# Optimization experiments

Measured on AMD Instinct MI355X. Metric: run time of the kernel, lower is better.

Reference implementation:

```python
import jax, jax.numpy as jnp
import numpy as np

EMBED = 1024
HEADS = 16
HEAD_DIM = EMBED // HEADS
B, T = 2, 2048
ROPE_THETA = 10000.0


def _rope(x):
    # x: [B, H, T, D]; standard half-split rotary embedding, applied per head
    D = x.shape[-1]
    inv_freq = 1.0 / (ROPE_THETA ** (jnp.arange(0, D, 2, dtype=jnp.float32) / D))  # [D/2]
    freqs = jnp.arange(x.shape[2], dtype=jnp.float32)[:, None] * inv_freq[None, :]  # [T, D/2]
    cos = jnp.cos(freqs).astype(x.dtype)  # [T, D/2]
    sin = jnp.sin(freqs).astype(x.dtype)
    x1, x2 = x[..., : D // 2], x[..., D // 2 :]
    return jnp.concatenate([x1 * cos - x2 * sin, x2 * cos + x1 * sin], axis=-1)


def setup_inputs() -> dict:
    key = jax.random.key(0)
    ks = jax.random.split(key, 5)
    s = 1.0 / np.sqrt(EMBED)
    return {
        "x": jax.random.normal(ks[0], (B, T, EMBED), dtype=jnp.float32),
        "Wq": jax.random.normal(ks[1], (EMBED, EMBED), dtype=jnp.float32) * s,
        "bq": jnp.zeros((EMBED,), dtype=jnp.float32),
        "Wk": jax.random.normal(ks[2], (EMBED, EMBED), dtype=jnp.float32) * s,
        "bk": jnp.zeros((EMBED,), dtype=jnp.float32),
        "Wv": jax.random.normal(ks[3], (EMBED, EMBED), dtype=jnp.float32) * s,
        "bv": jnp.zeros((EMBED,), dtype=jnp.float32),
        "Wo": jax.random.normal(ks[4], (EMBED, EMBED), dtype=jnp.float32) * s,
        "bo": jnp.zeros((EMBED,), dtype=jnp.float32),
    }


def reference(x, Wq, bq, Wk, bk, Wv, bv, Wo, bo):
    Bb, Tt, C = x.shape
    H, D = HEADS, HEAD_DIM
    # torch Linear: y = x @ W.T + b
    def proj(W, b):
        return (jnp.einsum("btc,oc->bto", x, W) + b).reshape(Bb, Tt, H, D).transpose(0, 2, 1, 3)

    q = _rope(proj(Wq, bq))  # [B, H, T, D]
    k = _rope(proj(Wk, bk))
    v = proj(Wv, bv)
    scale = jnp.sqrt(jnp.asarray(D, dtype=x.dtype))
    scores = jnp.einsum("bhtd,bhsd->bhts", q, k) / scale  # [B, H, T, T]
    attn = jax.nn.softmax(scores, axis=-1)  # dropout = identity in eval mode
    out = jnp.einsum("bhts,bhsd->bhtd", attn, v)  # [B, H, T, D]
    out = out.transpose(0, 2, 1, 3).reshape(Bb, Tt, C)
    return jnp.einsum("btc,oc->bto", out, Wo) + bo
```

## Files before the change

### kernel.cpp

```cpp
#include <hip/hip_runtime.h>
#include <hip/hip_bf16.h>

#define EMBED 1024
#define HEADS 16
#define HDIM 64
#define BATCH 2
#define SEQ 2048
#define MTOT (BATCH*SEQ)

typedef __attribute__((ext_vector_type(2))) float f32x2;
typedef __attribute__((ext_vector_type(4))) float f32x4;
typedef __attribute__((ext_vector_type(16))) float f32x16;
typedef __attribute__((ext_vector_type(4))) short s16x4;
typedef __attribute__((ext_vector_type(8))) short bf16x8;
typedef __attribute__((ext_vector_type(4))) int i32x4;

static __device__ __forceinline__ short f2bf(float f) {
  unsigned u = __builtin_bit_cast(unsigned, f);
  unsigned r = (u + 0x7fffu + ((u >> 16) & 1u)) >> 16;
  return (short)r;
}
static __device__ __forceinline__ float bf2f(short s) {
  unsigned u = ((unsigned)(unsigned short)s) << 16;
  return __builtin_bit_cast(float, u);
}
static __device__ __forceinline__ int pack2bf_fast(float lo, float hi) {
  unsigned ulo = __builtin_bit_cast(unsigned, lo) + 0x8000u;
  unsigned uhi = __builtin_bit_cast(unsigned, hi) + 0x8000u;
  int r;
  asm("v_cvt_pk_bf16_f32 %0, %1, %2" : "=v"(r)
      : "v"(__builtin_bit_cast(float, ulo)), "v"(__builtin_bit_cast(float, uhi)));
  return r;
}
static __device__ __forceinline__ void pswap(int &a, int &b) {
  asm("v_permlane32_swap_b32 %0, %1" : "+v"(a), "+v"(b));
}

typedef __attribute__((address_space(1))) const void gvoid_t;
typedef __attribute__((address_space(3))) void lvoid_t;
static __device__ __forceinline__ void gload_lds16(const void* g, void* l) {
  __builtin_amdgcn_global_load_lds((gvoid_t*)g, (lvoid_t*)l, 16, 0, 0);
}

__global__ __launch_bounds__(256) void cvt_bf16(
    const float* __restrict__ x,
    const float* __restrict__ Wq, const float* __restrict__ Wk,
    const float* __restrict__ Wv, const float* __restrict__ Wo,
    short* __restrict__ xb,
    short* __restrict__ Wqb, short* __restrict__ Wkb,
    short* __restrict__ Wvb, short* __restrict__ Wob,
    f32x2* __restrict__ tab)
{
  int i = blockIdx.x * 256 + threadIdx.x;
  if (i >= 2097152) {
    int i2 = i - 2097152;
    int t = i2 >> 5, j = i2 & 31;
    float invf = exp2f(-(float)j * 0.4152410118609203f);
    float sn, cs;
    sincosf((float)t * invf, &sn, &cs);
    f32x2 e; e[0] = cs; e[1] = sn;
    tab[i2] = e;
    return;
  }
  const float* src; short* dst; int off;
  if (i < 1048576) { src = x; dst = xb; off = i; }
  else {
    int j = i - 1048576;
    int w = j >> 18; off = j & 262143;
    src = (w == 0) ? Wq : (w == 1) ? Wk : (w == 2) ? Wv : Wo;
    dst = (w == 0) ? Wqb : (w == 1) ? Wkb : (w == 2) ? Wvb : Wob;
  }
  f32x4 v = ((const f32x4*)src)[off];
  s16x4 h;
#pragma unroll
  for (int j = 0; j < 4; ++j) h[j] = f2bf(v[j]);
  ((s16x4*)dst)[off] = h;
}

__global__ __launch_bounds__(256) void qkv_gemm(
    const short* __restrict__ xb,
    const short* __restrict__ Wqb, const short* __restrict__ Wkb, const short* __restrict__ Wvb,
    const float* __restrict__ bq, const float* __restrict__ bk, const float* __restrict__ bv,
    const f32x2* __restrict__ tab,
    short* __restrict__ Qb, short* __restrict__ Kb, short* __restrict__ Vb)
{
  __shared__ short As[128][64];
  __shared__ short Bs[128][64];
  int tid = threadIdx.x;
  int lane = tid & 63, wid = tid >> 6;
  int wm = wid >> 1, wn = wid & 1;
  int bm = blockIdx.x / 24;
  int bncol = blockIdx.x % 24;
  int wsel = bncol >> 3, bnn = bncol & 7;
  const short* W    = (wsel == 0) ? Wqb : (wsel == 1) ? Wkb : Wvb;
  const float* bias = (wsel == 0) ? bq : (wsel == 1) ? bk : bv;

  f32x4 acc[4][4] = {};

  const short* Abase = xb + (size_t)bm * 128 * EMBED;
  const short* Bbase = W + (size_t)bnn * 128 * EMBED;
  char* AsB = (char*)&As[0][0];
  char* BsB = (char*)&Bs[0][0];

  for (int kt = 0; kt < EMBED / 64; ++kt) {
#pragma unroll
    for (int i = 0; i < 4; ++i) {
      int s = tid + i * 256;
      int row = s >> 3, c = s & 7;
      int cs = c ^ (row & 7);
      gload_lds16(&Abase[(size_t)row * EMBED + kt * 64 + cs * 8],
                  AsB + i * 4096 + wid * 1024 + lane * 16);
      gload_lds16(&Bbase[(size_t)row * EMBED + kt * 64 + cs * 8],
                  BsB + i * 4096 + wid * 1024 + lane * 16);
    }
    __syncthreads();
#pragma unroll
    for (int kk = 0; kk < 2; ++kk) {
      int cp = ((kk * 4 + (lane >> 4)) ^ (lane & 7)) * 8;
      bf16x8 af[4], bfr[4];
#pragma unroll
      for (int mf = 0; mf < 4; ++mf)
        af[mf] = *(const bf16x8*)&As[wm * 64 + mf * 16 + (lane & 15)][cp];
#pragma unroll
      for (int nf = 0; nf < 4; ++nf)
        bfr[nf] = *(const bf16x8*)&Bs[wn * 64 + nf * 16 + (lane & 15)][cp];
      if (wsel == 2) {
#pragma unroll
        for (int mf = 0; mf < 4; ++mf)
#pragma unroll
          for (int nf = 0; nf < 4; ++nf)
            acc[mf][nf] = __builtin_amdgcn_mfma_f32_16x16x32_bf16(bfr[mf], af[nf], acc[mf][nf], 0, 0, 0);
      } else {
#pragma unroll
        for (int mf = 0; mf < 4; ++mf)
#pragma unroll
          for (int nf = 0; nf < 4; ++nf)
            acc[mf][nf] = __builtin_amdgcn_mfma_f32_16x16x32_bf16(af[mf], bfr[nf], acc[mf][nf], 0, 0, 0);
      }
    }
    __syncthreads();
  }

  if (wsel < 2) {
    short* dst = (wsel == 0) ? Qb : Kb;
    float sc = (wsel == 0) ? 0.18033688011112042f : 1.0f;
#pragma unroll
    for (int nf = 0; nf < 2; ++nf) {
      int col = bnn * 128 + wn * 64 + nf * 16 + (lane & 15);
      int h = col >> 6, j = col & 31;
      float b1 = bias[col], b2 = bias[col + 32];
#pragma unroll
      for (int mf = 0; mf < 4; ++mf) {
        int row0 = bm * 128 + wm * 64 + mf * 16 + ((lane >> 4) << 2);
#pragma unroll
        for (int r = 0; r < 4; ++r) {
          int m = row0 + r;
          int b_ = m >> 11, t = m & (SEQ - 1);
          f32x2 e = tab[t * 32 + j];
          float a1 = acc[mf][nf][r] + b1;
          float a2 = acc[mf][nf + 2][r] + b2;
          size_t o = (((size_t)(b_ * HEADS + h)) * SEQ + t) * HDIM + j;
          dst[o]      = f2bf((a1 * e[0] - a2 * e[1]) * sc);
          dst[o + 32] = f2bf((a2 * e[0] + a1 * e[1]) * sc);
        }
      }
    }
  } else {
#pragma unroll
    for (int mf = 0; mf < 4; ++mf) {
#pragma unroll
      for (int r = 0; r < 4; ++r) {
        int cch = bnn * 128 + wn * 64 + mf * 16 + ((lane >> 4) << 2) + r;
        int h = cch >> 6, d = cch & 63;
        float bb = bias[cch];
#pragma unroll
        for (int nf = 0; nf < 4; ++nf) {
          int m = bm * 128 + wm * 64 + nf * 16 + (lane & 15);
          int b_ = m >> 11, t = m & (SEQ - 1);
          Vb[((size_t)(b_ * HEADS + h) * HDIM + d) * SEQ + t] = f2bf(acc[mf][nf][r] + bb);
        }
      }
    }
  }
}

#define QBLK 128
#define KBLK 128

__global__ __launch_bounds__(256, 2) void attn_kernel(
    const short* __restrict__ Qb, const short* __restrict__ Kb,
    const short* __restrict__ Vb, short* __restrict__ Ob)
{
  __shared__ short Ks[KBLK][68];
  __shared__ short Vs[HDIM][132];

  int tid = threadIdx.x, lane = tid & 63, wid = tid >> 6;
  int l31 = lane & 31, lhi = lane >> 5;

  int bid = blockIdx.x;
  int swz = (bid & 7) * 64 + (bid >> 3);
  int qi = swz & 15, bh = swz >> 4;
  int b = bh >> 4, h = bh & 15;

  const short* Qp = Qb + ((size_t)bh * SEQ + qi * QBLK + wid * 32) * HDIM;
  const short* Kp = Kb + (size_t)bh * SEQ * HDIM;
  const short* Vp = Vb + (size_t)bh * HDIM * SEQ;

  bf16x8 qf[4];
#pragma unroll
  for (int cc = 0; cc < 4; ++cc)
    qf[cc] = *(const bf16x8*)&Qp[(size_t)l31 * HDIM + cc * 16 + lhi * 8];

  f32x16 oacc0 = {}, oacc1 = {}, lacc = {};
  bf16x8 vones;
#pragma unroll
  for (int j = 0; j < 8; ++j) vones[j] = (short)0x3F80;

  bf16x8 kreg[4], vreg[4];
#pragma unroll
  for (int i = 0; i < 4; ++i) {
    int s = tid + i * 256;
    kreg[i] = *(const bf16x8*)&Kp[(size_t)(s >> 3) * HDIM + (s & 7) * 8];
    vreg[i] = *(const bf16x8*)&Vp[(size_t)(s >> 4) * SEQ + (s & 15) * 8];
  }

  for (int kt = 0; kt < SEQ / KBLK; ++kt) {
#pragma unroll
    for (int i = 0; i < 4; ++i) {
      int s = tid + i * 256;
      *(bf16x8*)&Ks[s >> 3][(s & 7) * 8] = kreg[i];
      *(bf16x8*)&Vs[s >> 4][(s & 15) * 8] = vreg[i];
    }
    __syncthreads();

    if (kt + 1 < SEQ / KBLK) {
#pragma unroll
      for (int i = 0; i < 4; ++i) {
        int s = tid + i * 256;
        kreg[i] = *(const bf16x8*)&Kp[(size_t)((kt + 1) * KBLK + (s >> 3)) * HDIM + (s & 7) * 8];
        vreg[i] = *(const bf16x8*)&Vp[(size_t)(s >> 4) * SEQ + (kt + 1) * KBLK + (s & 15) * 8];
      }
    }

#pragma unroll
    for (int kbp = 0; kbp < 4; kbp += 2) {
      f32x16 s0 = {}, s1 = {};
      __builtin_amdgcn_s_setprio(1);
#pragma unroll
      for (int cc = 0; cc < 4; ++cc) {
        bf16x8 a0 = *(const bf16x8*)&Ks[(kbp + 0) * 32 + l31][cc * 16 + lhi * 8];
        bf16x8 a1 = *(const bf16x8*)&Ks[(kbp + 1) * 32 + l31][cc * 16 + lhi * 8];
        s0 = __builtin_amdgcn_mfma_f32_32x32x16_bf16(a0, qf[cc], s0, 0, 0, 0);
        s1 = __builtin_amdgcn_mfma_f32_32x32x16_bf16(a1, qf[cc], s1, 0, 0, 0);
      }
      __builtin_amdgcn_s_setprio(0);
      f32x16 p0, p1;
#pragma unroll
      for (int i = 0; i < 16; ++i) {
        p0[i] = __builtin_amdgcn_exp2f(s0[i]);
        p1[i] = __builtin_amdgcn_exp2f(s1[i]);
      }

#pragma unroll
      for (int c = 0; c < 2; ++c) {
        int w0 = pack2bf_fast(p0[8 * c + 0], p0[8 * c + 1]);
        int w1 = pack2bf_fast(p0[8 * c + 2], p0[8 * c + 3]);
        int w2 = pack2bf_fast(p0[8 * c + 4], p0[8 * c + 5]);
        int w3 = pack2bf_fast(p0[8 * c + 6], p0[8 * c + 7]);
        pswap(w0, w2);
        pswap(w1, w3);
        i32x4 pw; pw[0] = w0; pw[1] = w1; pw[2] = w2; pw[3] = w3;
        bf16x8 pa = __builtin_bit_cast(bf16x8, pw);

        bf16x8 vf0 = *(const bf16x8*)&Vs[l31][(kbp + 0) * 32 + c * 16 + lhi * 8];
        bf16x8 vf1 = *(const bf16x8*)&Vs[32 + l31][(kbp + 0) * 32 + c * 16 + lhi * 8];
        __builtin_amdgcn_s_setprio(1);
        lacc = __builtin_amdgcn_mfma_f32_32x32x16_bf16(pa, vones, lacc, 0, 0, 0);
        oacc0 = __builtin_amdgcn_mfma_f32_32x32x16_bf16(pa, vf0, oacc0, 0, 0, 0);
        oacc1 = __builtin_amdgcn_mfma_f32_32x32x16_bf16(pa, vf1, oacc1, 0, 0, 0);
        __builtin_amdgcn_s_setprio(0);
      }
#pragma unroll
      for (int c = 0; c < 2; ++c) {
        int w0 = pack2bf_fast(p1[8 * c + 0], p1[8 * c + 1]);
        int w1 = pack2bf_fast(p1[8 * c + 2], p1[8 * c + 3]);
        int w2 = pack2bf_fast(p1[8 * c + 4], p1[8 * c + 5]);
        int w3 = pack2bf_fast(p1[8 * c + 6], p1[8 * c + 7]);
        pswap(w0, w2);
        pswap(w1, w3);
        i32x4 pw; pw[0] = w0; pw[1] = w1; pw[2] = w2; pw[3] = w3;
        bf16x8 pa = __builtin_bit_cast(bf16x8, pw);

        bf16x8 vf0 = *(const bf16x8*)&Vs[l31][(kbp + 1) * 32 + c * 16 + lhi * 8];
        bf16x8 vf1 = *(const bf16x8*)&Vs[32 + l31][(kbp + 1) * 32 + c * 16 + lhi * 8];
        __builtin_amdgcn_s_setprio(1);
        lacc = __builtin_amdgcn_mfma_f32_32x32x16_bf16(pa, vones, lacc, 0, 0, 0);
        oacc0 = __builtin_amdgcn_mfma_f32_32x32x16_bf16(pa, vf0, oacc0, 0, 0, 0);
        oacc1 = __builtin_amdgcn_mfma_f32_32x32x16_bf16(pa, vf1, oacc1, 0, 0, 0);
        __builtin_amdgcn_s_setprio(0);
      }
    }
    __syncthreads();
  }

#pragma unroll
  for (int r = 0; r < 16; ++r) {
    int qrow = (r & 3) + 8 * (r >> 2) + 4 * lhi;
    int t = qi * QBLK + wid * 32 + qrow;
    float inv = 1.0f / lacc[r];
    size_t base = ((size_t)(b * SEQ + t)) * EMBED + h * HDIM;
    Ob[base + l31]      = f2bf(oacc0[r] * inv);
    Ob[base + 32 + l31] = f2bf(oacc1[r] * inv);
  }
}

__global__ __launch_bounds__(256) void out_gemm(
    const short* __restrict__ A, const short* __restrict__ Wob,
    const float* __restrict__ bo, float* __restrict__ C)
{
  __shared__ short As[64][64];
  __shared__ short Bs[128][64];
  int tid = threadIdx.x;
  int lane = tid & 63, wid = tid >> 6;
  int bm = blockIdx.x >> 3, bn = blockIdx.x & 7;

  f32x4 acc[8] = {};
  const short* Abase = A + (size_t)bm * 64 * EMBED;
  const short* Bbase = Wob + (size_t)bn * 128 * EMBED;
  char* AsB = (char*)&As[0][0];
  char* BsB = (char*)&Bs[0][0];

  for (int kt = 0; kt < EMBED / 64; ++kt) {
#pragma unroll
    for (int i = 0; i < 2; ++i) {
      int s = tid + i * 256;
      int row = s >> 3, c = s & 7;
      int cs = c ^ (row & 7);
      gload_lds16(&Abase[(size_t)row * EMBED + kt * 64 + cs * 8],
                  AsB + i * 4096 + wid * 1024 + lane * 16);
    }
#pragma unroll
    for (int i = 0; i < 4; ++i) {
      int s = tid + i * 256;
      int row = s >> 3, c = s & 7;
      int cs = c ^ (row & 7);
      gload_lds16(&Bbase[(size_t)row * EMBED + kt * 64 + cs * 8],
                  BsB + i * 4096 + wid * 1024 + lane * 16);
    }
    __syncthreads();
#pragma unroll
    for (int kk = 0; kk < 2; ++kk) {
      int cp = ((kk * 4 + (lane >> 4)) ^ (lane & 7)) * 8;
      bf16x8 af = *(const bf16x8*)&As[wid * 16 + (lane & 15)][cp];
#pragma unroll
      for (int nf = 0; nf < 8; ++nf) {
        bf16x8 bfr = *(const bf16x8*)&Bs[nf * 16 + (lane & 15)][cp];
        acc[nf] = __builtin_amdgcn_mfma_f32_16x16x32_bf16(af, bfr, acc[nf], 0, 0, 0);
      }
    }
    __syncthreads();
  }

#pragma unroll
  for (int nf = 0; nf < 8; ++nf) {
    int col = bn * 128 + nf * 16 + (lane & 15);
    float bb = bo[col];
    int row0 = bm * 64 + wid * 16 + ((lane >> 4) << 2);
#pragma unroll
    for (int r = 0; r < 4; ++r)
      C[(size_t)(row0 + r) * EMBED + col] = acc[nf][r] + bb;
  }
}

extern "C" void kernel_launch(void* const* d_in, const int* in_sizes, int n_in,
                              void* d_out, int out_size, void* d_ws, size_t ws_size,
                              hipStream_t stream) {
  const float* x  = (const float*)d_in[0];
  const float* Wq = (const float*)d_in[1];
  const float* bq = (const float*)d_in[2];
  const float* Wk = (const float*)d_in[3];
  const float* bk = (const float*)d_in[4];
  const float* Wv = (const float*)d_in[5];
  const float* bv = (const float*)d_in[6];
  const float* Wo = (const float*)d_in[7];
  const float* bo = (const float*)d_in[8];
  float* out = (float*)d_out;
  char* ws = (char*)d_ws;

  const size_t MB = 1u << 20;
  short* Qb  = (short*)(ws);
  short* Kb  = (short*)(ws + 8 * MB);
  short* Vb  = (short*)(ws + 16 * MB);
  short* XOb = (short*)(ws + 24 * MB);
  short* Wqb = (short*)(ws + 32 * MB);
  short* Wkb = (short*)(ws + 34 * MB);
  short* Wvb = (short*)(ws + 36 * MB);
  short* Wob = (short*)(ws + 38 * MB);
  f32x2* tab = (f32x2*)(ws + 40 * MB);

  cvt_bf16<<<dim3(8448), dim3(256), 0, stream>>>(x, Wq, Wk, Wv, Wo, XOb, Wqb, Wkb, Wvb, Wob, tab);
  qkv_gemm<<<dim3(32 * 24), dim3(256), 0, stream>>>(XOb, Wqb, Wkb, Wvb, bq, bk, bv, tab, Qb, Kb, Vb);
  attn_kernel<<<dim3(BATCH * HEADS * (SEQ / QBLK)), dim3(256), 0, stream>>>(Qb, Kb, Vb, XOb);
  out_gemm<<<dim3(64 * 8), dim3(256), 0, stream>>>(XOb, Wob, bo, out);
}
```

Measured before the change: 121.0 us.

## Double-buffer K/V shared tiles with 64-key blocks and one barrier per tile

Shrinks the attention key block from 128 to 64 and double-buffers the K and V shared-memory tiles. Each iteration computes from the current buffer and writes the prefetched next tile into the other buffer, which leaves one barrier per iteration instead of two. It also drops the s_setprio hints around the MFMA groups. The cost is twice as many loop iterations, each with fewer MFMAs to hide global-load latency behind.

```diff
diff --git a/kernel.cpp b/kernel.cpp
--- a/kernel.cpp
+++ b/kernel.cpp
@@ -185,14 +185,14 @@
 }
 
 #define QBLK 128
-#define KBLK 128
+#define KBLK 64
 
 __global__ __launch_bounds__(256, 2) void attn_kernel(
     const short* __restrict__ Qb, const short* __restrict__ Kb,
     const short* __restrict__ Vb, short* __restrict__ Ob)
 {
-  __shared__ short Ks[KBLK][68];
-  __shared__ short Vs[HDIM][132];
+  __shared__ short Ks[2][KBLK][68];
+  __shared__ short Vs[2][HDIM][68];
 
   int tid = threadIdx.x, lane = tid & 63, wid = tid >> 6;
   int l31 = lane & 31, lhi = lane >> 5;
@@ -216,91 +216,91 @@
 #pragma unroll
   for (int j = 0; j < 8; ++j) vones[j] = (short)0x3F80;
 
-  bf16x8 kreg[4], vreg[4];
-#pragma unroll
-  for (int i = 0; i < 4; ++i) {
+  bf16x8 kreg[2], vreg[2];
+#pragma unroll
+  for (int i = 0; i < 2; ++i) {
     int s = tid + i * 256;
     kreg[i] = *(const bf16x8*)&Kp[(size_t)(s >> 3) * HDIM + (s & 7) * 8];
-    vreg[i] = *(const bf16x8*)&Vp[(size_t)(s >> 4) * SEQ + (s & 15) * 8];
-  }
+    vreg[i] = *(const bf16x8*)&Vp[(size_t)(s >> 3) * SEQ + (s & 7) * 8];
+  }
+#pragma unroll
+  for (int i = 0; i < 2; ++i) {
+    int s = tid + i * 256;
+    *(bf16x8*)&Ks[0][s >> 3][(s & 7) * 8] = kreg[i];
+    *(bf16x8*)&Vs[0][s >> 3][(s & 7) * 8] = vreg[i];
+  }
+  __syncthreads();
 
   for (int kt = 0; kt < SEQ / KBLK; ++kt) {
-#pragma unroll
-    for (int i = 0; i < 4; ++i) {
-      int s = tid + i * 256;
-      *(bf16x8*)&Ks[s >> 3][(s & 7) * 8] = kreg[i];
-      *(bf16x8*)&Vs[s >> 4][(s & 15) * 8] = vreg[i];
-    }
-    __syncthreads();
-
+    int cur = kt & 1;
     if (kt + 1 < SEQ / KBLK) {
 #pragma unroll
-      for (int i = 0; i < 4; ++i) {
+      for (int i = 0; i < 2; ++i) {
         int s = tid + i * 256;
         kreg[i] = *(const bf16x8*)&Kp[(size_t)((kt + 1) * KBLK + (s >> 3)) * HDIM + (s & 7) * 8];
-        vreg[i] = *(const bf16x8*)&Vp[(size_t)(s >> 4) * SEQ + (kt + 1) * KBLK + (s & 15) * 8];
-      }
-    }
-
-#pragma unroll
-    for (int kbp = 0; kbp < 4; kbp += 2) {
-      f32x16 s0 = {}, s1 = {};
-      __builtin_amdgcn_s_setprio(1);
-#pragma unroll
-      for (int cc = 0; cc < 4; ++cc) {
-        bf16x8 a0 = *(const bf16x8*)&Ks[(kbp + 0) * 32 + l31][cc * 16 + lhi * 8];
-        bf16x8 a1 = *(const bf16x8*)&Ks[(kbp + 1) * 32 + l31][cc * 16 + lhi * 8];
-        s0 = __builtin_amdgcn_mfma_f32_32x32x16_bf16(a0, qf[cc], s0, 0, 0, 0);
-        s1 = __builtin_amdgcn_mfma_f32_32x32x16_bf16(a1, qf[cc], s1, 0, 0, 0);
-      }
-      __builtin_amdgcn_s_setprio(0);
-      f32x16 p0, p1;
-#pragma unroll
-      for (int i = 0; i < 16; ++i) {
-        p0[i] = __builtin_amdgcn_exp2f(s0[i]);
-        p1[i] = __builtin_amdgcn_exp2f(s1[i]);
-      }
-
-#pragma unroll
-      for (int c = 0; c < 2; ++c) {
-        int w0 = pack2bf_fast(p0[8 * c + 0], p0[8 * c + 1]);
-        int w1 = pack2bf_fast(p0[8 * c + 2], p0[8 * c + 3]);
-        int w2 = pack2bf_fast(p0[8 * c + 4], p0[8 * c + 5]);
-        int w3 = pack2bf_fast(p0[8 * c + 6], p0[8 * c + 7]);
-        pswap(w0, w2);
-        pswap(w1, w3);
-        i32x4 pw; pw[0] = w0; pw[1] = w1; pw[2] = w2; pw[3] = w3;
-        bf16x8 pa = __builtin_bit_cast(bf16x8, pw);
-
-        bf16x8 vf0 = *(const bf16x8*)&Vs[l31][(kbp + 0) * 32 + c * 16 + lhi * 8];
-        bf16x8 vf1 = *(const bf16x8*)&Vs[32 + l31][(kbp + 0) * 32 + c * 16 + lhi * 8];
-        __builtin_amdgcn_s_setprio(1);
-        lacc = __builtin_amdgcn_mfma_f32_32x32x16_bf16(pa, vones, lacc, 0, 0, 0);
-        oacc0 = __builtin_amdgcn_mfma_f32_32x32x16_bf16(pa, vf0, oacc0, 0, 0, 0);
-        oacc1 = __builtin_amdgcn_mfma_f32_32x32x16_bf16(pa, vf1, oacc1, 0, 0, 0);
-        __builtin_amdgcn_s_setprio(0);
-      }
-#pragma unroll
-      for (int c = 0; c < 2; ++c) {
-        int w0 = pack2bf_fast(p1[8 * c + 0], p1[8 * c + 1]);
-        int w1 = pack2bf_fast(p1[8 * c + 2], p1[8 * c + 3]);
-        int w2 = pack2bf_fast(p1[8 * c + 4], p1[8 * c + 5]);
-        int w3 = pack2bf_fast(p1[8 * c + 6], p1[8 * c + 7]);
-        pswap(w0, w2);
-        pswap(w1, w3);
-        i32x4 pw; pw[0] = w0; pw[1] = w1; pw[2] = w2; pw[3] = w3;
-        bf16x8 pa = __builtin_bit_cast(bf16x8, pw);
-
-        bf16x8 vf0 = *(const bf16x8*)&Vs[l31][(kbp + 1) * 32 + c * 16 + lhi * 8];
-        bf16x8 vf1 = *(const bf16x8*)&Vs[32 + l31][(kbp + 1) * 32 + c * 16 + lhi * 8];
-        __builtin_amdgcn_s_setprio(1);
-        lacc = __builtin_amdgcn_mfma_f32_32x32x16_bf16(pa, vones, lacc, 0, 0, 0);
-        oacc0 = __builtin_amdgcn_mfma_f32_32x32x16_bf16(pa, vf0, oacc0, 0, 0, 0);
-        oacc1 = __builtin_amdgcn_mfma_f32_32x32x16_bf16(pa, vf1, oacc1, 0, 0, 0);
-        __builtin_amdgcn_s_setprio(0);
-      }
-    }
-    __syncthreads();
+        vreg[i] = *(const bf16x8*)&Vp[(size_t)(s >> 3) * SEQ + (kt + 1) * KBLK + (s & 7) * 8];
+      }
+    }
+
+    f32x16 s0 = {}, s1 = {};
+#pragma unroll
+    for (int cc = 0; cc < 4; ++cc) {
+      bf16x8 a0 = *(const bf16x8*)&Ks[cur][l31][cc * 16 + lhi * 8];
+      bf16x8 a1 = *(const bf16x8*)&Ks[cur][32 + l31][cc * 16 + lhi * 8];
+      s0 = __builtin_amdgcn_mfma_f32_32x32x16_bf16(a0, qf[cc], s0, 0, 0, 0);
+      s1 = __builtin_amdgcn_mfma_f32_32x32x16_bf16(a1, qf[cc], s1, 0, 0, 0);
+    }
+    f32x16 p0, p1;
+#pragma unroll
+    for (int i = 0; i < 16; ++i) {
+      p0[i] = __builtin_amdgcn_exp2f(s0[i]);
+      p1[i] = __builtin_amdgcn_exp2f(s1[i]);
+    }
+
+#pragma unroll
+    for (int c = 0; c < 2; ++c) {
+      int w0 = pack2bf_fast(p0[8 * c + 0], p0[8 * c + 1]);
+      int w1 = pack2bf_fast(p0[8 * c + 2], p0[8 * c + 3]);
+      int w2 = pack2bf_fast(p0[8 * c + 4], p0[8 * c + 5]);
+      int w3 = pack2bf_fast(p0[8 * c + 6], p0[8 * c + 7]);
+      pswap(w0, w2);
+      pswap(w1, w3);
+      i32x4 pw; pw[0] = w0; pw[1] = w1; pw[2] = w2; pw[3] = w3;
+      bf16x8 pa = __builtin_bit_cast(bf16x8, pw);
+
+      bf16x8 vf0 = *(const bf16x8*)&Vs[cur][l31][c * 16 + lhi * 8];
+      bf16x8 vf1 = *(const bf16x8*)&Vs[cur][32 + l31][c * 16 + lhi * 8];
+      lacc = __builtin_amdgcn_mfma_f32_32x32x16_bf16(pa, vones, lacc, 0, 0, 0);
+      oacc0 = __builtin_amdgcn_mfma_f32_32x32x16_bf16(pa, vf0, oacc0, 0, 0, 0);
+      oacc1 = __builtin_amdgcn_mfma_f32_32x32x16_bf16(pa, vf1, oacc1, 0, 0, 0);
+    }
+#pragma unroll
+    for (int c = 0; c < 2; ++c) {
+      int w0 = pack2bf_fast(p1[8 * c + 0], p1[8 * c + 1]);
+      int w1 = pack2bf_fast(p1[8 * c + 2], p1[8 * c + 3]);
+      int w2 = pack2bf_fast(p1[8 * c + 4], p1[8 * c + 5]);
+      int w3 = pack2bf_fast(p1[8 * c + 6], p1[8 * c + 7]);
+      pswap(w0, w2);
+      pswap(w1, w3);
+      i32x4 pw; pw[0] = w0; pw[1] = w1; pw[2] = w2; pw[3] = w3;
+      bf16x8 pa = __builtin_bit_cast(bf16x8, pw);
+
+      bf16x8 vf0 = *(const bf16x8*)&Vs[cur][l31][32 + c * 16 + lhi * 8];
+      bf16x8 vf1 = *(const bf16x8*)&Vs[cur][32 + l31][32 + c * 16 + lhi * 8];
+      lacc = __builtin_amdgcn_mfma_f32_32x32x16_bf16(pa, vones, lacc, 0, 0, 0);
+      oacc0 = __builtin_amdgcn_mfma_f32_32x32x16_bf16(pa, vf0, oacc0, 0, 0, 0);
+      oacc1 = __builtin_amdgcn_mfma_f32_32x32x16_bf16(pa, vf1, oacc1, 0, 0, 0);
+    }
+
+    if (kt + 1 < SEQ / KBLK) {
+#pragma unroll
+      for (int i = 0; i < 2; ++i) {
+        int s = tid + i * 256;
+        *(bf16x8*)&Ks[cur ^ 1][s >> 3][(s & 7) * 8] = kreg[i];
+        *(bf16x8*)&Vs[cur ^ 1][s >> 3][(s & 7) * 8] = vreg[i];
+      }
+      __syncthreads();
+    }
   }
 
 #pragma unroll
```

After: 118.8 us. Within noise of the previous version (-1.8%).
